# Kernel tuning notes

Hardware: AMD Instinct MI355X
Metric: run time of the kernel (lower is better)

The kernel has to match this reference:

```python
import jax, jax.numpy as jnp
import numpy as np

B, E, H, W, P, C = 2, 256, 192, 192, 16, 80
GRIDS = (40, 36, 24, 16, 12)
L = len(GRIDS)
MASK_W, CLS_W, ALPHA, GAMMA, EPS = 3.0, 1.0, 0.25, 2.0, 1e-4


def setup_inputs() -> dict:
    key = jax.random.key(0)
    ks = jax.random.split(key, 32)
    inp = {"mask_out": jax.random.normal(ks[0], (B, E, H, W), jnp.float32)}
    for i, g in enumerate(GRIDS):
        inp[f"kernel_l{i}"] = jax.random.normal(ks[1 + i], (B, g, g, E), jnp.float32) * 0.05
        inp[f"cate_l{i}"] = jax.random.uniform(ks[6 + i], (B, g, g, C), jnp.float32)
        inp[f"pos_l{i}"] = jax.random.randint(ks[11 + i], (B, P), 0, g * g, dtype=jnp.int32)
        inp[f"cate_t_l{i}"] = jax.random.randint(ks[16 + i], (B, g, g), -1, C, dtype=jnp.int32)
    # binary instance masks, image-major layout [B, L, P, H, W]
    inp["mask_targets"] = (jax.random.uniform(ks[21], (B, L, P, H, W)) > 0.9).astype(jnp.float32)
    return inp


def _forward(mask_out, kernels, cates, mask_targets, pos_idxs, cate_ts):
    # --- dynamic 1x1 conv: gather positive kernels and apply as batched matmul ---
    preds = []
    for kl, pl in zip(kernels, pos_idxs):
        g2 = kl.shape[1] * kl.shape[2]
        kflat = kl.reshape(B, g2, E)
        kp = jnp.take_along_axis(kflat, pl[:, :, None], axis=1)  # [B, P, E]
        preds.append(jnp.einsum('bpe,behw->bphw', kp, mask_out))  # F.conv2d 1x1
    preds = jnp.stack(preds)  # [L, B, P, H, W]  (level-major, matches torch cat order)

    # --- dice loss ---
    mp = jax.nn.sigmoid(preds).reshape(L * B * P, H * W)
    # NOTE: original code concatenates targets image-major (img, level) while preds
    # are level-major (level, img); we reproduce that pairing faithfully.
    mt = mask_targets.reshape(B * L * P, H * W)
    a = jnp.sum(mp * mt, axis=1)
    b = jnp.sum(mp * mp, axis=1)
    c = jnp.sum(mt * mt, axis=1)
    mask_loss = jnp.sum(1.0 - 2.0 * a / (b + c + 1e-4)) / (L * B * P)

    # --- focal loss on positive grid cells ---
    tgt = jnp.concatenate([t.reshape(-1) for t in cate_ts])            # [N]
    prd = jnp.concatenate([cl.reshape(-1, C) for cl in cates])          # [N, C]
    posm = (tgt > -1).astype(jnp.float32)
    p = jnp.clip(prd, EPS, 1.0 - EPS)
    gt = jax.nn.one_hot(jnp.clip(tgt, 0, C - 1), C, dtype=jnp.float32)
    af = jnp.where(gt == 1.0, ALPHA, 1.0 - ALPHA)
    pt = jnp.where(gt == 1.0, p, 1.0 - p)
    fw = af * (1.0 - pt) ** GAMMA
    ce = -(gt * jnp.log(p) + (1.0 - gt) * jnp.log(1.0 - p))
    cls_loss = jnp.sum(fw * ce * posm[:, None]) / jnp.sum(posm)

    return jnp.stack([MASK_W * mask_loss, CLS_W * cls_loss])  # [mask_loss, cls_loss]


def reference(mask_out, kernel_l0, kernel_l1, kernel_l2, kernel_l3, kernel_l4,
              cate_l0, cate_l1, cate_l2, cate_l3, cate_l4, mask_targets,
              pos_l0, pos_l1, pos_l2, pos_l3, pos_l4,
              cate_t_l0, cate_t_l1, cate_t_l2, cate_t_l3, cate_t_l4):
    return _forward(mask_out,
                    (kernel_l0, kernel_l1, kernel_l2, kernel_l3, kernel_l4),
                    (cate_l0, cate_l1, cate_l2, cate_l3, cate_l4),
                    mask_targets,
                    (pos_l0, pos_l1, pos_l2, pos_l3, pos_l4),
                    (cate_t_l0, cate_t_l1, cate_t_l2, cate_t_l3, cate_t_l4))
```

## Files before the change

### kernel.cpp

```cpp
#include <hip/hip_runtime.h>
#include <hip/hip_bf16.h>

namespace {

constexpr int kHW = 36864;

typedef __attribute__((ext_vector_type(8))) short bf16x8;
typedef __attribute__((ext_vector_type(4))) float f32x4;

__device__ __forceinline__ unsigned short f2bf(float x) {
  return __builtin_bit_cast(unsigned short, __float2bfloat16(x));
}
__device__ __forceinline__ float bf2f(unsigned short u) {
  return __builtin_bit_cast(float, (unsigned int)u << 16);
}

__device__ __forceinline__ float wave_sum(float v) {
#pragma unroll
  for (int off = 32; off; off >>= 1) v += __shfl_xor(v, off, 64);
  return v;
}

__global__ __launch_bounds__(256) void prep_kernel(
    const float* __restrict__ k0, const float* __restrict__ k1,
    const float* __restrict__ k2, const float* __restrict__ k3,
    const float* __restrict__ k4,
    const int* __restrict__ q0, const int* __restrict__ q1,
    const int* __restrict__ q2, const int* __restrict__ q3,
    const int* __restrict__ q4,
    unsigned short* __restrict__ kbf, float* __restrict__ acc) {
  const int bid = blockIdx.x;
  if (bid == 0) {
    for (int i = threadIdx.x; i < 482; i += 256) acc[i] = 0.f;
    return;
  }
  const int idx = bid - 1;
  const int b = idx / 80;
  const int row = idx - b * 80;
  if (threadIdx.x >= 128) return;
  const int l = row >> 4, p = row & 15;
  const float* kb[5] = {k0, k1, k2, k3, k4};
  const int* pb[5] = {q0, q1, q2, q3, q4};
  const int bg2[5] = {b * 1600, b * 1296, b * 576, b * 256, b * 144};
  const int pos = pb[l][b * 16 + p];
  const int ch = threadIdx.x * 2;
  const float2 kv = *(const float2*)(kb[l] + (size_t)(bg2[l] + pos) * 256 + ch);
  *(unsigned int*)&kbf[((size_t)b * 80 + row) * 256 + ch] =
      (unsigned int)f2bf(kv.x) | ((unsigned int)f2bf(kv.y) << 16);
}

__global__ __attribute__((amdgpu_flat_work_group_size(256, 256),
                          amdgpu_waves_per_eu(2, 4)))
void gemm_store_kernel(const float* __restrict__ mask_out,
                       const unsigned short* __restrict__ kbf,
                       unsigned short* __restrict__ predw) {
  const int bid = blockIdx.x;
  const int b = bid / 576;
  const int tile = bid - b * 576;
  const int px0 = tile * 64;
  const int lane = threadIdx.x & 63;
  const int wv = threadIdx.x >> 6;
  const int px16 = lane & 15;
  const int hi8 = (lane >> 4) * 8;
  const int pxl = px0 + wv * 16 + px16;

  const float* __restrict__ mo =
      mask_out + (size_t)b * 256 * kHW + (size_t)hi8 * kHW + pxl;

  float br[8][8];
#pragma unroll
  for (int ks = 0; ks < 8; ++ks)
#pragma unroll
    for (int j = 0; j < 8; ++j)
      br[ks][j] = mo[(size_t)(ks * 32 + j) * kHW];

#pragma unroll
  for (int ks = 0; ks < 8; ++ks)
#pragma unroll
    for (int j = 0; j < 8; ++j) asm volatile("" : "+v"(br[ks][j]));

  const unsigned short* __restrict__ ka =
      kbf + ((size_t)b * 80 + px16) * 256 + hi8;

  f32x4 a5[5];
#pragma unroll
  for (int mt = 0; mt < 5; ++mt) a5[mt] = (f32x4){0.f, 0.f, 0.f, 0.f};

#pragma unroll
  for (int ks = 0; ks < 8; ++ks) {
    bf16x8 bb;
#pragma unroll
    for (int j = 0; j < 8; ++j) bb[j] = (short)f2bf(br[ks][j]);
#pragma unroll
    for (int mt = 0; mt < 5; ++mt) {
      const bf16x8 af = *(const bf16x8*)(ka + mt * 4096 + ks * 32);
      a5[mt] =
          __builtin_amdgcn_mfma_f32_16x16x32_bf16(af, bb, a5[mt], 0, 0, 0);
    }
  }

#pragma unroll
  for (int mt = 0; mt < 5; ++mt) {
#pragma unroll
    for (int j = 0; j < 4; ++j) {
      const int row80 = mt * 16 + (lane >> 4) * 4 + j;
      const int r = (row80 >> 4) * 32 + b * 16 + (row80 & 15);
      predw[(size_t)r * kHW + pxl] = f2bf(a5[mt][j]);
    }
  }
}

__global__ __launch_bounds__(256) void dice_kernel(
    const unsigned short* __restrict__ predw,
    const float* __restrict__ mtg, float* __restrict__ acc) {
  const int r = blockIdx.x / 18;
  const int cb = blockIdx.x - r * 18;
  const int px = cb * 2048 + threadIdx.x * 8;
  const size_t base = (size_t)r * kHW + px;
  const bf16x8 p8 = *(const bf16x8*)&predw[base];
  const float4 t0 = *(const float4*)&mtg[base];
  const float4 t1 = *(const float4*)&mtg[base + 4];
  const float tv[8] = {t0.x, t0.y, t0.z, t0.w, t1.x, t1.y, t1.z, t1.w};
  float av = 0.f, bv = 0.f, cv = 0.f;
#pragma unroll
  for (int j = 0; j < 8; ++j) {
    const float x = bf2f((unsigned short)p8[j]);
    const float mp = 1.f / (1.f + __expf(-x));
    av = fmaf(mp, tv[j], av);
    bv = fmaf(mp, mp, bv);
    cv += tv[j];
  }
  av = wave_sum(av);
  bv = wave_sum(bv);
  cv = wave_sum(cv);
  __shared__ float st[12];
  const int w = threadIdx.x >> 6;
  if ((threadIdx.x & 63) == 0) {
    st[w] = av;
    st[4 + w] = bv;
    st[8 + w] = cv;
  }
  __syncthreads();
  if (threadIdx.x < 3) {
    const int q = threadIdx.x;
    unsafeAtomicAdd(&acc[q * 160 + r], st[q * 4] + st[q * 4 + 1] +
                                           st[q * 4 + 2] + st[q * 4 + 3]);
  }
}

__global__ __launch_bounds__(256) void focal_kernel(
    const float* __restrict__ c0, const float* __restrict__ c1,
    const float* __restrict__ c2, const float* __restrict__ c3,
    const float* __restrict__ c4,
    const int* __restrict__ t0, const int* __restrict__ t1,
    const int* __restrict__ t2, const int* __restrict__ t3,
    const int* __restrict__ t4,
    float* __restrict__ acc) {
  const int idx = blockIdx.x * 256 + threadIdx.x;
  const int n = idx / 20;
  const int cq = (idx - n * 20) * 4;
  int t;
  const float* crow;
  if (n < 3200) {
    t = t0[n]; crow = c0 + (size_t)n * 80;
  } else if (n < 5792) {
    const int o = n - 3200; t = t1[o]; crow = c1 + (size_t)o * 80;
  } else if (n < 6944) {
    const int o = n - 5792; t = t2[o]; crow = c2 + (size_t)o * 80;
  } else if (n < 7456) {
    const int o = n - 6944; t = t3[o]; crow = c3 + (size_t)o * 80;
  } else {
    const int o = n - 7456; t = t4[o]; crow = c4 + (size_t)o * 80;
  }
  float term = 0.f, np = 0.f;
  if (t > -1) {
    const float4 pv4 = *(const float4*)&crow[cq];
    const float pvs[4] = {pv4.x, pv4.y, pv4.z, pv4.w};
#pragma unroll
    for (int j = 0; j < 4; ++j) {
      float pv = fminf(fmaxf(pvs[j], 1e-4f), 1.f - 1e-4f);
      const bool gm = (cq + j == t);
      const float af = gm ? 0.25f : 0.75f;
      const float pt = gm ? pv : 1.f - pv;
      const float om = 1.f - pt;
      term = fmaf(af * om * om, -__logf(pt), term);
    }
    if (cq == 0) np = 1.f;
  }
  term = wave_sum(term);
  np = wave_sum(np);
  __shared__ float st[8];
  const int wid = threadIdx.x >> 6;
  if ((threadIdx.x & 63) == 0) {
    st[wid] = term;
    st[4 + wid] = np;
  }
  __syncthreads();
  if (threadIdx.x == 0) {
    unsafeAtomicAdd(&acc[480], st[0] + st[1] + st[2] + st[3]);
    unsafeAtomicAdd(&acc[481], st[4] + st[5] + st[6] + st[7]);
  }
}

__global__ __launch_bounds__(64) void finalize_kernel(
    const float* __restrict__ acc, float* __restrict__ out) {
  const int tid = threadIdx.x;
  float s = 0.f;
#pragma unroll
  for (int rr = 0; rr < 3; ++rr) {
    const int r = tid + rr * 64;
    if (r < 160) {
      const float a = acc[r];
      const float bb = acc[160 + r];
      const float cc = acc[320 + r];
      s += 1.f - 2.f * a / (bb + cc + 1e-4f);
    }
  }
  s = wave_sum(s);
  if (tid == 0) {
    out[0] = 3.0f * (s / 160.f);
    out[1] = acc[480] / acc[481];
  }
}

}

extern "C" void kernel_launch(void* const* d_in, const int* in_sizes, int n_in,
                              void* d_out, int out_size, void* d_ws,
                              size_t ws_size, hipStream_t stream) {
  const float* mask_out = (const float*)d_in[0];
  const float* k[5];
  const float* cc[5];
  const int* pp[5];
  const int* tt[5];
  for (int i = 0; i < 5; ++i) {
    k[i] = (const float*)d_in[1 + 4 * i];
    cc[i] = (const float*)d_in[2 + 4 * i];
    pp[i] = (const int*)d_in[3 + 4 * i];
    tt[i] = (const int*)d_in[4 + 4 * i];
  }
  const float* mt = (const float*)d_in[21];

  char* ws = (char*)d_ws;
  float* acc = (float*)ws;
  unsigned short* kbf = (unsigned short*)(ws + 8192);
  unsigned short* predw = (unsigned short*)(ws + 90112);
  float* out = (float*)d_out;

  hipLaunchKernelGGL(prep_kernel, dim3(161), dim3(256), 0, stream, k[0], k[1],
                     k[2], k[3], k[4], pp[0], pp[1], pp[2], pp[3], pp[4], kbf,
                     acc);
  hipLaunchKernelGGL(gemm_store_kernel, dim3(1152), dim3(256), 0, stream,
                     mask_out, kbf, predw);
  hipLaunchKernelGGL(dice_kernel, dim3(160 * 18), dim3(256), 0, stream, predw,
                     mt, acc);
  hipLaunchKernelGGL(focal_kernel, dim3(605), dim3(256), 0, stream, cc[0],
                     cc[1], cc[2], cc[3], cc[4], tt[0], tt[1], tt[2], tt[3],
                     tt[4], acc);
  hipLaunchKernelGGL(finalize_kernel, dim3(1), dim3(64), 0, stream, acc, out);
}
```

Measured before the change: 74.55 us.

## Stage GEMM B operand via direct global-to-LDS loads and fuse dice/focal kernels

The GEMM kernel now copies the mask_out tile into a 64KB shared buffer with global_load_lds, then reads B fragments from LDS, instead of holding 64 floats per thread in registers. The aim is to cut register pressure and get wider, coalesced global loads. Separately, the dice and focal reduction kernels are merged into one launch with a block-index split, removing one kernel launch. The large LDS footprint limits occupancy, and the column-strided LDS reads may cause bank conflicts.

```diff
diff --git a/kernel.cpp b/kernel.cpp
--- a/kernel.cpp
+++ b/kernel.cpp
@@ -4,6 +4,8 @@
 namespace {
 
 constexpr int kHW = 36864;
+constexpr int kDiceBlocks = 2880;
+constexpr int kFocalBlocks = 605;
 
 typedef __attribute__((ext_vector_type(8))) short bf16x8;
 typedef __attribute__((ext_vector_type(4))) float f32x4;
@@ -49,11 +51,12 @@
       (unsigned int)f2bf(kv.x) | ((unsigned int)f2bf(kv.y) << 16);
 }
 
-__global__ __attribute__((amdgpu_flat_work_group_size(256, 256),
-                          amdgpu_waves_per_eu(2, 4)))
-void gemm_store_kernel(const float* __restrict__ mask_out,
-                       const unsigned short* __restrict__ kbf,
-                       unsigned short* __restrict__ predw) {
+__global__ __launch_bounds__(256, 2) void gemm_store_kernel(
+    const float* __restrict__ mask_out,
+    const unsigned short* __restrict__ kbf,
+    unsigned short* __restrict__ predw) {
+  __shared__ float bufB[256][64];
+
   const int bid = blockIdx.x;
   const int b = bid / 576;
   const int tile = bid - b * 576;
@@ -64,20 +67,20 @@
   const int hi8 = (lane >> 4) * 8;
   const int pxl = px0 + wv * 16 + px16;
 
-  const float* __restrict__ mo =
-      mask_out + (size_t)b * 256 * kHW + (size_t)hi8 * kHW + pxl;
-
-  float br[8][8];
-#pragma unroll
-  for (int ks = 0; ks < 8; ++ks)
-#pragma unroll
-    for (int j = 0; j < 8; ++j)
-      br[ks][j] = mo[(size_t)(ks * 32 + j) * kHW];
-
-#pragma unroll
-  for (int ks = 0; ks < 8; ++ks)
-#pragma unroll
-    for (int j = 0; j < 8; ++j) asm volatile("" : "+v"(br[ks][j]));
+  const float* __restrict__ gstage = mask_out + (size_t)b * 256 * kHW +
+                                     (size_t)(wv * 4 + (lane >> 4)) * kHW +
+                                     px0 + (lane & 15) * 4;
+#pragma unroll
+  for (int i = 0; i < 16; ++i) {
+    __builtin_amdgcn_global_load_lds(
+        (const __attribute__((address_space(1))) unsigned int*)(gstage +
+                                                                (size_t)i * 16 *
+                                                                    kHW),
+        (__attribute__((address_space(3))) unsigned int*)&bufB[i * 16 + wv * 4]
+            [0],
+        16, 0, 0);
+  }
+  __syncthreads();
 
   const unsigned short* __restrict__ ka =
       kbf + ((size_t)b * 80 + px16) * 256 + hi8;
@@ -88,9 +91,12 @@
 
 #pragma unroll
   for (int ks = 0; ks < 8; ++ks) {
+    float fb[8];
+#pragma unroll
+    for (int j = 0; j < 8; ++j) fb[j] = bufB[ks * 32 + hi8 + j][wv * 16 + px16];
     bf16x8 bb;
 #pragma unroll
-    for (int j = 0; j < 8; ++j) bb[j] = (short)f2bf(br[ks][j]);
+    for (int j = 0; j < 8; ++j) bb[j] = (short)f2bf(fb[j]);
 #pragma unroll
     for (int mt = 0; mt < 5; ++mt) {
       const bf16x8 af = *(const bf16x8*)(ka + mt * 4096 + ks * 32);
@@ -110,45 +116,8 @@
   }
 }
 
-__global__ __launch_bounds__(256) void dice_kernel(
-    const unsigned short* __restrict__ predw,
-    const float* __restrict__ mtg, float* __restrict__ acc) {
-  const int r = blockIdx.x / 18;
-  const int cb = blockIdx.x - r * 18;
-  const int px = cb * 2048 + threadIdx.x * 8;
-  const size_t base = (size_t)r * kHW + px;
-  const bf16x8 p8 = *(const bf16x8*)&predw[base];
-  const float4 t0 = *(const float4*)&mtg[base];
-  const float4 t1 = *(const float4*)&mtg[base + 4];
-  const float tv[8] = {t0.x, t0.y, t0.z, t0.w, t1.x, t1.y, t1.z, t1.w};
-  float av = 0.f, bv = 0.f, cv = 0.f;
-#pragma unroll
-  for (int j = 0; j < 8; ++j) {
-    const float x = bf2f((unsigned short)p8[j]);
-    const float mp = 1.f / (1.f + __expf(-x));
-    av = fmaf(mp, tv[j], av);
-    bv = fmaf(mp, mp, bv);
-    cv += tv[j];
-  }
-  av = wave_sum(av);
-  bv = wave_sum(bv);
-  cv = wave_sum(cv);
-  __shared__ float st[12];
-  const int w = threadIdx.x >> 6;
-  if ((threadIdx.x & 63) == 0) {
-    st[w] = av;
-    st[4 + w] = bv;
-    st[8 + w] = cv;
-  }
-  __syncthreads();
-  if (threadIdx.x < 3) {
-    const int q = threadIdx.x;
-    unsafeAtomicAdd(&acc[q * 160 + r], st[q * 4] + st[q * 4 + 1] +
-                                           st[q * 4 + 2] + st[q * 4 + 3]);
-  }
-}
-
-__global__ __launch_bounds__(256) void focal_kernel(
+__global__ __launch_bounds__(256) void dice_focal_kernel(
+    const unsigned short* __restrict__ predw, const float* __restrict__ mtg,
     const float* __restrict__ c0, const float* __restrict__ c1,
     const float* __restrict__ c2, const float* __restrict__ c3,
     const float* __restrict__ c4,
@@ -156,7 +125,46 @@
     const int* __restrict__ t2, const int* __restrict__ t3,
     const int* __restrict__ t4,
     float* __restrict__ acc) {
-  const int idx = blockIdx.x * 256 + threadIdx.x;
+  const int bid = blockIdx.x;
+  __shared__ float st[12];
+
+  if (bid < kDiceBlocks) {
+    const int r = bid / 18;
+    const int cb = bid - r * 18;
+    const int px = cb * 2048 + threadIdx.x * 8;
+    const size_t base = (size_t)r * kHW + px;
+    const bf16x8 p8 = *(const bf16x8*)&predw[base];
+    const float4 u0 = *(const float4*)&mtg[base];
+    const float4 u1 = *(const float4*)&mtg[base + 4];
+    const float tv[8] = {u0.x, u0.y, u0.z, u0.w, u1.x, u1.y, u1.z, u1.w};
+    float av = 0.f, bv = 0.f, cv = 0.f;
+#pragma unroll
+    for (int j = 0; j < 8; ++j) {
+      const float x = bf2f((unsigned short)p8[j]);
+      const float mp = 1.f / (1.f + __expf(-x));
+      av = fmaf(mp, tv[j], av);
+      bv = fmaf(mp, mp, bv);
+      cv += tv[j];
+    }
+    av = wave_sum(av);
+    bv = wave_sum(bv);
+    cv = wave_sum(cv);
+    const int w = threadIdx.x >> 6;
+    if ((threadIdx.x & 63) == 0) {
+      st[w] = av;
+      st[4 + w] = bv;
+      st[8 + w] = cv;
+    }
+    __syncthreads();
+    if (threadIdx.x < 3) {
+      const int q = threadIdx.x;
+      unsafeAtomicAdd(&acc[q * 160 + r], st[q * 4] + st[q * 4 + 1] +
+                                             st[q * 4 + 2] + st[q * 4 + 3]);
+    }
+    return;
+  }
+
+  const int idx = (bid - kDiceBlocks) * 256 + threadIdx.x;
   const int n = idx / 20;
   const int cq = (idx - n * 20) * 4;
   int t;
@@ -189,7 +197,6 @@
   }
   term = wave_sum(term);
   np = wave_sum(np);
-  __shared__ float st[8];
   const int wid = threadIdx.x >> 6;
   if ((threadIdx.x & 63) == 0) {
     st[wid] = term;
@@ -252,10 +259,8 @@
                      acc);
   hipLaunchKernelGGL(gemm_store_kernel, dim3(1152), dim3(256), 0, stream,
                      mask_out, kbf, predw);
-  hipLaunchKernelGGL(dice_kernel, dim3(160 * 18), dim3(256), 0, stream, predw,
-                     mt, acc);
-  hipLaunchKernelGGL(focal_kernel, dim3(605), dim3(256), 0, stream, cc[0],
-                     cc[1], cc[2], cc[3], cc[4], tt[0], tt[1], tt[2], tt[3],
-                     tt[4], acc);
+  hipLaunchKernelGGL(dice_focal_kernel, dim3(kDiceBlocks + kFocalBlocks),
+                     dim3(256), 0, stream, predw, mt, cc[0], cc[1], cc[2],
+                     cc[3], cc[4], tt[0], tt[1], tt[2], tt[3], tt[4], acc);
   hipLaunchKernelGGL(finalize_kernel, dim3(1), dim3(64), 0, stream, acc, out);
 }
```

Measured after the change: 72.45 us. 2.8% less time.
